# Kernel optimization log

Measured on AMD Instinct MI355X. Metric: run time of the kernel, lower is better.

The kernel has to match this reference:

```python
import jax, jax.numpy as jnp
import numpy as np

DN = ('NHWC', 'HWIO', 'NHWC')
EPS = 1e-3  # Keras BatchNormalization default epsilon


def conv2d(x, w):
    return jax.lax.conv_general_dilated(x, w, (1, 1), 'SAME', dimension_numbers=DN)


def hard_sigmoid(x):
    # Keras ConvLSTM2D default recurrent_activation
    return jnp.clip(0.2 * x + 0.5, 0.0, 1.0)


def convlstm2d(x, Wx, Wh, b):
    """Keras ConvLSTM2D, return_sequences=True. x: (B,T,H,W,C).
    Wx: (3,3,C,4F) input kernel, Wh: (3,3,F,4F) recurrent kernel, b: (4F,).
    Gate order (Keras): i, f, c, o."""
    B, T, H, W, C = x.shape
    F = Wh.shape[2]
    # input-to-gate convs for all timesteps in one batched conv
    xg = conv2d(x.reshape(B * T, H, W, C), Wx) + b          # (B*T,H,W,4F)
    xg = xg.reshape(B, T, H, W, 4 * F).transpose(1, 0, 2, 3, 4)  # (T,B,H,W,4F)

    def step(carry, xg_t):
        h, c = carry
        g = xg_t + conv2d(h, Wh)                            # (B,H,W,4F)
        i, f, cc, o = jnp.split(g, 4, axis=-1)
        i = hard_sigmoid(i)
        f = hard_sigmoid(f)
        o = hard_sigmoid(o)
        c = f * c + i * jnp.tanh(cc)
        h = o * jnp.tanh(c)
        return (h, c), h

    h0 = jnp.zeros((B, H, W, F), x.dtype)
    (_, _), hs = jax.lax.scan(step, (h0, h0), xg)           # hs: (T,B,H,W,F)
    return hs.transpose(1, 0, 2, 3, 4)


def batchnorm(x, gamma, beta):
    # training-mode BN over all axes except channel (last)
    mu = x.mean(axis=(0, 1, 2, 3), keepdims=True)
    var = x.var(axis=(0, 1, 2, 3), keepdims=True)
    return gamma * (x - mu) * jax.lax.rsqrt(var + EPS) + beta


def setup_inputs() -> dict:
    key = jax.random.key(0)
    B, T, H, W, C = 4, 8, 16, 16, 256
    F = 256
    ks = jax.random.split(key, 10)
    s = 0.02
    inp = {
        'input_tensor': jax.random.normal(ks[0], (B, T, H, W, C), jnp.float32),
        'Wx1': jax.random.normal(ks[1], (3, 3, C, 4 * F), jnp.float32) * s,
        'Wh1': jax.random.normal(ks[2], (3, 3, F, 4 * F), jnp.float32) * s,
        'b1': jnp.zeros((4 * F,), jnp.float32),
        'g1': jnp.ones((F,), jnp.float32),
        'be1': jnp.zeros((F,), jnp.float32),
        'Wx2': jax.random.normal(ks[3], (3, 3, F, 4 * F), jnp.float32) * s,
        'Wh2': jax.random.normal(ks[4], (3, 3, F, 4 * F), jnp.float32) * s,
        'b2': jnp.zeros((4 * F,), jnp.float32),
        'g2': jnp.ones((F,), jnp.float32),
        'be2': jnp.zeros((F,), jnp.float32),
        'Wx3': jax.random.normal(ks[5], (3, 3, F, 4 * F), jnp.float32) * s,
        'Wh3': jax.random.normal(ks[6], (3, 3, F, 4 * F), jnp.float32) * s,
        'b3': jnp.zeros((4 * F,), jnp.float32),
        'g3': jnp.ones((F,), jnp.float32),
        'be3': jnp.zeros((F,), jnp.float32),
    }
    return inp


def reference(input_tensor, Wx1, Wh1, b1, g1, be1,
              Wx2, Wh2, b2, g2, be2,
              Wx3, Wh3, b3, g3, be3):
    x = batchnorm(convlstm2d(input_tensor, Wx1, Wh1, b1), g1, be1)
    x = batchnorm(convlstm2d(x, Wx2, Wh2, b2), g2, be2)
    x = batchnorm(convlstm2d(x, Wx3, Wh3, b3), g3, be3)
    return x
```

## Files before the change

kernel.cpp:

```cpp
#include <hip/hip_runtime.h>

#define HW      256
#define COUT    1024
#define TSTEPS  8
#define BN_EPS  1e-3f
#define KTOT    2304

typedef unsigned short u16;
typedef unsigned int   u32;
typedef __attribute__((ext_vector_type(8))) _Float16 v8h;
typedef __attribute__((ext_vector_type(4))) float v4f;

__device__ __forceinline__ u16 f2h(float x) {
    _Float16 h = (_Float16)x; return *(u16*)&h;
}
__device__ __forceinline__ float h2f(u16 u) {
    _Float16 h = *(_Float16*)&u; return (float)h;
}
__device__ __forceinline__ float hsig(float x) {
    return fminf(fmaxf(0.2f * x + 0.5f, 0.f), 1.f);
}

typedef __attribute__((address_space(1))) const unsigned int gas_u32;
typedef __attribute__((address_space(3))) unsigned int las_u32;
__device__ __forceinline__ void gl16(const void* g, void* l) {
    __builtin_amdgcn_global_load_lds((gas_u32*)g, (las_u32*)l, 16, 0, 0);
}

__global__ __launch_bounds__(256, 2) void conv_big_k(
    const u16* __restrict__ apad,
    const u16* __restrict__ wT,
    const float* __restrict__ bias,
    u16* __restrict__ out)
{
    constexpr int KQ = 36;
    __shared__ u16 lds[2 * 16384];

    const int bid = blockIdx.x;
    const int xcd = bid & 7, idx = bid >> 3;
    const int by = (xcd >> 1) * 2 + (idx & 1);
    const int bx = (xcd & 1) * 32 + (idx >> 1);
    const int m0 = bx * 128, n0 = by * 128;
    const int tid = threadIdx.x, lane = tid & 63, w = tid >> 6;
    const int wr = w >> 1, wc = w & 1;
    const int lr = lane >> 3;
    const int g  = (lane & 7) ^ lr;
    const int fr = lane & 15, kc = lane >> 4;

    const char* a_src[4];
    #pragma unroll
    for (int i = 0; i < 4; ++i) {
        int m = m0 + w * 32 + i * 8 + lr;
        int img = m >> 8, pix = m & 255, yy = pix >> 4, xx = pix & 15;
        a_src[i] = (const char*)apad + ((((long)img * 18 + yy) * 18 + xx) * 256 + g * 8) * 2;
    }
    const char* b_src[4];
    #pragma unroll
    for (int i = 0; i < 4; ++i) {
        int n = n0 + w * 32 + i * 8 + lr;
        b_src[i] = (const char*)wT + ((long)n * KTOT + g * 8) * 2;
    }

    int aro[4][2], bro[4][2];
    #pragma unroll
    for (int mi = 0; mi < 4; ++mi) {
        int rl = wr * 64 + mi * 16 + fr;
        #pragma unroll
        for (int ks = 0; ks < 2; ++ks)
            aro[mi][ks] = rl * 128 + ((((ks << 2) | kc) ^ (fr & 7)) << 4);
    }
    #pragma unroll
    for (int ni = 0; ni < 4; ++ni) {
        int nr = wc * 64 + ni * 16 + fr;
        #pragma unroll
        for (int ks = 0; ks < 2; ++ks)
            bro[ni][ks] = 16384 + nr * 128 + ((((ks << 2) | kc) ^ (fr & 7)) << 4);
    }

    v4f acc[4][4];
    #pragma unroll
    for (int mi = 0; mi < 4; ++mi)
        #pragma unroll
        for (int ni = 0; ni < 4; ++ni) acc[mi][ni] = (v4f)0.f;

#define STAGE_B(J) { int j_ = (J); int dxy = j_ >> 2, c64 = j_ & 3;           \
    int dy = (dxy * 11) >> 5; int dx = dxy - dy * 3;                          \
    int aoff = ((dy * 18 + dx) * 256 + c64 * 64) * 2; int boff = j_ * 128;    \
    char* base = (char*)lds + (j_ & 1) * 32768;                               \
    _Pragma("unroll") for (int i = 0; i < 4; ++i)                             \
        gl16(a_src[i] + aoff, base + (w * 32 + i * 8) * 128);                 \
    _Pragma("unroll") for (int i = 0; i < 4; ++i)                             \
        gl16(b_src[i] + boff, base + 16384 + (w * 32 + i * 8) * 128); }

#define COMPUTE_B(J) { const char* base = (const char*)lds + ((J) & 1) * 32768; \
    v8h af[4][2], bf[4][2];                                                   \
    _Pragma("unroll") for (int mi = 0; mi < 4; ++mi)                          \
        _Pragma("unroll") for (int ks = 0; ks < 2; ++ks)                      \
            af[mi][ks] = *(const v8h*)(base + aro[mi][ks]);                   \
    _Pragma("unroll") for (int ni = 0; ni < 4; ++ni)                          \
        _Pragma("unroll") for (int ks = 0; ks < 2; ++ks)                      \
            bf[ni][ks] = *(const v8h*)(base + bro[ni][ks]);                   \
    __builtin_amdgcn_s_setprio(1);                                            \
    _Pragma("unroll") for (int ks = 0; ks < 2; ++ks)                          \
    _Pragma("unroll") for (int mi = 0; mi < 4; ++mi)                          \
    _Pragma("unroll") for (int ni = 0; ni < 4; ++ni)                          \
        acc[mi][ni] = __builtin_amdgcn_mfma_f32_16x16x32_f16(af[mi][ks], bf[ni][ks], acc[mi][ni], 0, 0, 0); \
    __builtin_amdgcn_s_setprio(0); }

    STAGE_B(0);
    for (int kq = 0; kq < KQ - 1; ++kq) {
        asm volatile("s_waitcnt vmcnt(0)" ::: "memory");
        __builtin_amdgcn_s_barrier();
        __builtin_amdgcn_sched_barrier(0);
        STAGE_B(kq + 1);
        COMPUTE_B(kq);
    }
    asm volatile("s_waitcnt vmcnt(0)" ::: "memory");
    __builtin_amdgcn_s_barrier();
    __builtin_amdgcn_sched_barrier(0);
    COMPUTE_B(KQ - 1);
#undef STAGE_B
#undef COMPUTE_B

    #pragma unroll
    for (int mi = 0; mi < 4; ++mi) {
        #pragma unroll
        for (int ni = 0; ni < 4; ++ni) {
            int mrow = m0 + wr * 64 + mi * 16 + ((lane >> 4) << 2);
            int ncol = n0 + wc * 64 + ni * 16 + fr;
            float b0 = bias[(ncol & 3) * 256 + (ncol >> 2)];
            #pragma unroll
            for (int r = 0; r < 4; ++r)
                out[(long)(mrow + r) * COUT + ncol] = f2h(acc[mi][ni][r] + b0);
        }
    }
}

__global__ __launch_bounds__(512) void rec_fused_k(
    const u16* __restrict__ ph_in,
    const u16* __restrict__ wTf,
    const u16* __restrict__ xg,
    float* __restrict__ cbuf,
    float* __restrict__ hs,
    u16* __restrict__ ph_out,
    int t)
{
    __shared__ u16 lds[6 * 4096];

    const int bid = blockIdx.x;
    const int by = (bid & 7) * 2 + ((bid >> 3) & 1);
    const int bx = bid >> 4;
    const int m0 = bx * 64, n0 = by * 64;
    const int tid = threadIdx.x, lane = tid & 63, w = tid >> 6;
    const int wr = w >> 2, wc = w & 3;
    const int fr = lane & 15, kc = lane >> 4;

    const int f4  = n0 + wc * 16 + (lane & 12);
    const int fch = f4 >> 2;
    int erow[2]; long xrow[2];
    uint2 xb_pre[2];
    #pragma unroll
    for (int mi = 0; mi < 2; ++mi) {
        erow[mi] = m0 + wr * 32 + mi * 16 + ((lane >> 4) << 2) + (lane & 3);
        int img = erow[mi] >> 8, pix = erow[mi] & 255;
        xrow[mi] = ((long)(img * TSTEPS + t) * HW + pix);
        xb_pre[mi] = *(const uint2*)&xg[xrow[mi] * COUT + f4];
    }

    const char* a_src;
    {
        int rt = tid >> 3;
        int gg = (tid & 7) ^ (rt & 7);
        int m = m0 + rt;
        int img = m >> 8, pix = m & 255, yy = pix >> 4, xx = pix & 15;
        a_src = (const char*)ph_in + ((((long)img * 18 + yy) * 18 + xx) * 256 + gg * 8) * 2;
    }
    const char* b_base = (const char*)wTf + ((long)(by * 4 + wc) * 72) * 1024 + lane * 16;

    int aro[2][2];
    #pragma unroll
    for (int mi = 0; mi < 2; ++mi)
        #pragma unroll
        for (int ks = 0; ks < 2; ++ks)
            aro[mi][ks] = (wr * 32 + mi * 16 + fr) * 128 + ((((ks << 2) | kc) ^ (fr & 7)) << 4);

    v4f acc0 = (v4f)0.f, acc1 = (v4f)0.f;

#define STAGE_A(J, BUF) { int j_ = (J); int dxy = j_ >> 2, c64 = j_ & 3;      \
    int dy = (dxy * 11) >> 5; int dx = dxy - dy * 3;                          \
    int aoff = ((dy * 18 + dx) * 256 + c64 * 64) * 2;                         \
    gl16(a_src + aoff, (char*)lds + (BUF) * 8192 + w * 1024); }

#define LDB(J, R0, R1) { R0 = *(const v8h*)(b_base + (2 * (J)) * 1024);       \
                         R1 = *(const v8h*)(b_base + (2 * (J) + 1) * 1024); }

#define CKQ(BUF, C0, C1) {                                                    \
    const char* base_ = (const char*)lds + (BUF) * 8192;                      \
    v8h af00_ = *(const v8h*)(base_ + aro[0][0]);                             \
    v8h af10_ = *(const v8h*)(base_ + aro[1][0]);                             \
    v8h af01_ = *(const v8h*)(base_ + aro[0][1]);                             \
    v8h af11_ = *(const v8h*)(base_ + aro[1][1]);                             \
    __builtin_amdgcn_s_setprio(1);                                            \
    acc0 = __builtin_amdgcn_mfma_f32_16x16x32_f16(af00_, C0, acc0, 0, 0, 0);  \
    acc1 = __builtin_amdgcn_mfma_f32_16x16x32_f16(af10_, C0, acc1, 0, 0, 0);  \
    acc0 = __builtin_amdgcn_mfma_f32_16x16x32_f16(af01_, C1, acc0, 0, 0, 0);  \
    acc1 = __builtin_amdgcn_mfma_f32_16x16x32_f16(af11_, C1, acc1, 0, 0, 0);  \
    __builtin_amdgcn_s_setprio(0); }

#define BODY2(J2, BC, BS, Ca0, Ca1, Cb0, Cb1, La0, La1, Lb0, Lb1) {           \
    int q0_ = 2 * (J2);                                                       \
    asm volatile("s_waitcnt vmcnt(6)" ::: "memory");                          \
    __builtin_amdgcn_s_barrier();                                             \
    __builtin_amdgcn_sched_barrier(0);                                        \
    LDB(q0_ + 4, La0, La1); LDB(q0_ + 5, Lb0, Lb1);                           \
    STAGE_A(q0_ + 4, BS); STAGE_A(q0_ + 5, (BS) + 1);                         \
    CKQ(BC,       Ca0, Ca1);                                                  \
    CKQ((BC) + 1, Cb0, Cb1); }

    v8h S00, S01, S02, S03, S10, S11, S12, S13, S20, S21, S22, S23;
    LDB(0, S00, S01); LDB(1, S02, S03); STAGE_A(0, 0); STAGE_A(1, 1);
    LDB(2, S10, S11); LDB(3, S12, S13); STAGE_A(2, 2); STAGE_A(3, 3);

    for (int j = 0; j < 5; ++j) {
        BODY2(3 * j,     0, 4, S00, S01, S02, S03, S20, S21, S22, S23);
        BODY2(3 * j + 1, 2, 0, S10, S11, S12, S13, S00, S01, S02, S03);
        BODY2(3 * j + 2, 4, 2, S20, S21, S22, S23, S10, S11, S12, S13);
    }
    BODY2(15, 0, 4, S00, S01, S02, S03, S20, S21, S22, S23);
    asm volatile("s_waitcnt vmcnt(6)" ::: "memory");
    __builtin_amdgcn_s_barrier();
    __builtin_amdgcn_sched_barrier(0);
    CKQ(2, S10, S11);
    CKQ(3, S12, S13);
    asm volatile("s_waitcnt vmcnt(0)" ::: "memory");
    __builtin_amdgcn_s_barrier();
    __builtin_amdgcn_sched_barrier(0);
    CKQ(4, S20, S21);
    CKQ(5, S22, S23);
#undef STAGE_A
#undef LDB
#undef CKQ
#undef BODY2

    v4f accA[2] = {acc0, acc1};
    const bool gl0 = lane & 1, gl1 = lane & 2;
    #pragma unroll
    for (int mi = 0; mi < 2; ++mi) {
        float V0 = accA[mi][0], V1 = accA[mi][1];
        float V2 = accA[mi][2], V3 = accA[mi][3];
        float x0 = __shfl_xor(V0, 1), x1 = __shfl_xor(V1, 1);
        float x2 = __shfl_xor(V2, 1), x3 = __shfl_xor(V3, 1);
        float a0 = gl0 ? x1 : V0;
        float a1 = gl0 ? V1 : x0;
        float a2 = gl0 ? x3 : V2;
        float a3 = gl0 ? V3 : x2;
        float s0 = __shfl_xor(a0, 2), s1 = __shfl_xor(a1, 2);
        float s2 = __shfl_xor(a2, 2), s3 = __shfl_xor(a3, 2);
        float Ti = gl1 ? s2 : a0;
        float Tf = gl1 ? s3 : a1;
        float Tc = gl1 ? a2 : s0;
        float To = gl1 ? a3 : s1;

        float pi = Ti + h2f((u16)(xb_pre[mi].x & 0xffff));
        float pf = Tf + h2f((u16)(xb_pre[mi].x >> 16));
        float pc = Tc + h2f((u16)(xb_pre[mi].y & 0xffff));
        float po = To + h2f((u16)(xb_pre[mi].y >> 16));
        long cidx = (long)erow[mi] * 256 + fch;
        float c = hsig(pf) * cbuf[cidx] + hsig(pi) * tanhf(pc);
        float h = hsig(po) * tanhf(c);
        cbuf[cidx] = c;
        hs[xrow[mi] * 256 + fch] = h;
        int pix = erow[mi] & 255, img = erow[mi] >> 8;
        ph_out[(((long)img * 18 + (pix >> 4) + 1) * 18 + (pix & 15) + 1) * 256 + fch] = f2h(h);
    }
}

__global__ __launch_bounds__(256) void gates0_k(
    const u16* __restrict__ xg, float* __restrict__ cbuf,
    float* __restrict__ hs, u16* __restrict__ ph_out)
{
    int idx = blockIdx.x * 256 + threadIdx.x;
    int fch = idx & 255, row = idx >> 8;
    int img = row >> 8, pix = row & 255;
    long xrow = (long)(img * TSTEPS) * HW + pix;
    uint2 xb = *(const uint2*)&xg[xrow * COUT + fch * 4];
    float pi = h2f((u16)(xb.x & 0xffff));
    float pc = h2f((u16)(xb.y & 0xffff));
    float po = h2f((u16)(xb.y >> 16));
    float c = hsig(pi) * tanhf(pc);
    float h = hsig(po) * tanhf(c);
    cbuf[(long)row * 256 + fch] = c;
    hs[xrow * 256 + fch] = h;
    int yy = pix >> 4, xx = pix & 15;
    ph_out[(((long)img * 18 + yy + 1) * 18 + xx + 1) * 256 + fch] = f2h(h);
}

__global__ __launch_bounds__(256) void wprep_all_k(
    const float* __restrict__ wx, const float* __restrict__ wh,
    u16* __restrict__ wT, u16* __restrict__ wTf)
{
    int kq = blockIdx.x;
    int by = blockIdx.y;
    if (by < 4) {
        int k0 = kq * 32;
        int np = by * 256 + threadIdx.x;
        int n  = (np & 3) * 256 + (np >> 2);
        u32 pk[16];
        #pragma unroll
        for (int kk = 0; kk < 32; kk += 2) {
            float a = wx[(long)(k0 + kk) * COUT + n];
            float b = wx[(long)(k0 + kk + 1) * COUT + n];
            pk[kk >> 1] = (u32)f2h(a) | ((u32)f2h(b) << 16);
        }
        uint4* dst = (uint4*)&wT[(long)np * KTOT + k0];
        dst[0] = make_uint4(pk[0], pk[1], pk[2], pk[3]);
        dst[1] = make_uint4(pk[4], pk[5], pk[6], pk[7]);
        dst[2] = make_uint4(pk[8], pk[9], pk[10], pk[11]);
        dst[3] = make_uint4(pk[12], pk[13], pk[14], pk[15]);
    } else {
        int nf = (by - 4) * 4 + (threadIdx.x >> 6);
        int l  = threadIdx.x & 63;
        int np = nf * 16 + (l & 15);
        int n  = (np & 3) * 256 + (np >> 2);
        int k0 = kq * 32 + (l >> 4) * 8;
        u32 pk[4];
        #pragma unroll
        for (int e = 0; e < 8; e += 2) {
            float a = wh[(long)(k0 + e) * COUT + n];
            float b = wh[(long)(k0 + e + 1) * COUT + n];
            pk[e >> 1] = (u32)f2h(a) | ((u32)f2h(b) << 16);
        }
        *(uint4*)&wTf[((long)(nf * 72) + kq) * 512 + l * 8] =
            make_uint4(pk[0], pk[1], pk[2], pk[3]);
    }
}

__global__ __launch_bounds__(256) void convert_x_k(const float* __restrict__ x,
                                                   u16* __restrict__ padx)
{
    int q = blockIdx.x * 256 + threadIdx.x;
    int e0 = q * 4;
    int f = e0 & 255, pix = (e0 >> 8) & 255, img = e0 >> 16;
    float4 v = ((const float4*)x)[q];
    int yy = pix >> 4, xx = pix & 15;
    long o = (((long)img * 18 + yy + 1) * 18 + xx + 1) * 256 + f;
    u32 lo = (u32)f2h(v.x) | ((u32)f2h(v.y) << 16);
    u32 hi = (u32)f2h(v.z) | ((u32)f2h(v.w) << 16);
    *(uint2*)&padx[o] = make_uint2(lo, hi);
}

__global__ __launch_bounds__(256) void bn_stats1_k(
    const float* __restrict__ x, float* __restrict__ partial)
{
    const int tid = threadIdx.x;
    const int blk = blockIdx.x;
    float s = 0.f, s2 = 0.f;
    const long base = (long)blk * 128 * 256;
    #pragma unroll 8
    for (int gi = 0; gi < 128; ++gi) {
        float v = x[base + gi * 256 + tid];
        s += v; s2 += v * v;
    }
    partial[blk * 512 + tid]       = s;
    partial[blk * 512 + 256 + tid] = s2;
}

__global__ __launch_bounds__(256) void bn_stats2_k(
    const float* __restrict__ partial, const float* __restrict__ gamma,
    const float* __restrict__ beta, float* __restrict__ stats)
{
    const int f = threadIdx.x;
    float s = 0.f, s2 = 0.f;
    #pragma unroll 8
    for (int b = 0; b < 64; ++b) {
        s  += partial[b * 512 + f];
        s2 += partial[b * 512 + 256 + f];
    }
    const float inv_n = 1.f / 8192.f;
    float mu  = s * inv_n;
    float var = s2 * inv_n - mu * mu;
    float sc  = gamma[f] * rsqrtf(var + BN_EPS);
    stats[f]       = sc;
    stats[256 + f] = beta[f] - mu * sc;
}

__global__ __launch_bounds__(256) void bn_apply_k(
    const float* __restrict__ x, const float* __restrict__ stats,
    u16* __restrict__ padx, float* __restrict__ out)
{
    const int q = blockIdx.x * 256 + threadIdx.x;
    const int e0 = q * 4;
    const int f = e0 & 255, pix = (e0 >> 8) & 255, img = e0 >> 16;
    float4 v  = ((const float4*)x)[q];
    float4 sc = *(const float4*)(stats + f);
    float4 sh = *(const float4*)(stats + 256 + f);
    v.x = v.x * sc.x + sh.x;
    v.y = v.y * sc.y + sh.y;
    v.z = v.z * sc.z + sh.z;
    v.w = v.w * sc.w + sh.w;
    if (out) ((float4*)out)[q] = v;
    if (padx) {
        int yy = pix >> 4, xx = pix & 15;
        long o = (((long)img * 18 + yy + 1) * 18 + xx + 1) * 256 + f;
        u32 lo = (u32)f2h(v.x) | ((u32)f2h(v.y) << 16);
        u32 hi = (u32)f2h(v.z) | ((u32)f2h(v.w) << 16);
        *(uint2*)&padx[o] = make_uint2(lo, hi);
    }
}

extern "C" void kernel_launch(void* const* d_in, const int* in_sizes, int n_in,
                              void* d_out, int out_size, void* d_ws, size_t ws_size,
                              hipStream_t stream)
{
    const float* x0    = (const float*)d_in[0];
    const float* Wx[3] = {(const float*)d_in[1], (const float*)d_in[6],  (const float*)d_in[11]};
    const float* Wh[3] = {(const float*)d_in[2], (const float*)d_in[7],  (const float*)d_in[12]};
    const float* bb[3] = {(const float*)d_in[3], (const float*)d_in[8],  (const float*)d_in[13]};
    const float* gg[3] = {(const float*)d_in[4], (const float*)d_in[9],  (const float*)d_in[14]};
    const float* be[3] = {(const float*)d_in[5], (const float*)d_in[10], (const float*)d_in[15]};

    float* ws    = (float*)d_ws;
    u16*  xg     = (u16*)ws;
    float* cbuf  = ws   + 4194304;
    float* hs    = cbuf + 262144;
    float* part  = hs   + 2097152;
    float* stats = part + 262144;
    u16*  pad_x  = (u16*)(stats + 512);
    u16*  pad_h  = pad_x + 2654208;
    u16*  wTx    = pad_h + 663552;
    u16*  wTf    = wTx   + 2359296;
    const long PHN = 331776;

    hipMemsetAsync(pad_x, 0, 2654208 * sizeof(u16), stream);
    hipMemsetAsync(pad_h, 0, 2 * PHN * sizeof(u16), stream);
    hipLaunchKernelGGL(convert_x_k, dim3(2048), dim3(256), 0, stream, x0, pad_x);

    for (int l = 0; l < 3; ++l) {
        hipLaunchKernelGGL(wprep_all_k, dim3(72, 20), dim3(256), 0, stream,
            Wx[l], Wh[l], wTx, wTf);

        hipLaunchKernelGGL(conv_big_k, dim3(512), dim3(256), 0, stream,
            pad_x, wTx, bb[l], xg);

        hipLaunchKernelGGL(gates0_k, dim3(1024), dim3(256), 0, stream,
            xg, cbuf, hs, pad_h + PHN);

        for (int t = 1; t < TSTEPS; ++t) {
            hipLaunchKernelGGL(rec_fused_k, dim3(256), dim3(512), 0, stream,
                pad_h + (t & 1) * PHN, wTf, xg, cbuf, hs,
                pad_h + ((t & 1) ^ 1) * PHN, t);
        }

        hipLaunchKernelGGL(bn_stats1_k, dim3(64), dim3(256), 0, stream, hs, part);
        hipLaunchKernelGGL(bn_stats2_k, dim3(1), dim3(256), 0, stream, part, gg[l], be[l], stats);
        hipLaunchKernelGGL(bn_apply_k, dim3(2048), dim3(256), 0, stream, hs, stats,
            (l < 2) ? pad_x : (u16*)nullptr, (l == 2) ? (float*)d_out : (float*)nullptr);
    }
}
```

Baseline: 471.3 us.

## Fuse t=0 gate computation into input conv epilogue and store hidden states in fp16

Removes the separate gates0 kernel by computing the first timestep's LSTM cell and hidden state inside the conv_big epilogue for blocks whose rows belong to t=0. The hidden-state sequence buffer changes from fp32 to fp16, which halves traffic in the BN stats and apply kernels. The BN stats partial grid is rebalanced to 128 blocks. The recurrent kernel also loads the previous cell state before the GEMM. The fp16 hidden-state storage slightly reduces the precision of the BN inputs.

```diff
diff --git a/kernel.cpp b/kernel.cpp
--- a/kernel.cpp
+++ b/kernel.cpp
@@ -31,7 +31,10 @@
     const u16* __restrict__ apad,
     const u16* __restrict__ wT,
     const float* __restrict__ bias,
-    u16* __restrict__ out)
+    u16* __restrict__ out,
+    float* __restrict__ cbuf,
+    u16* __restrict__ hs16,
+    u16* __restrict__ ph1)
 {
     constexpr int KQ = 36;
     __shared__ u16 lds[2 * 16384];
@@ -122,6 +125,8 @@
 #undef STAGE_B
 #undef COMPUTE_B
 
+    const bool t0blk = (((m0 >> 8) & 7) == 0);
+    const bool gl0 = lane & 1, gl1 = lane & 2;
     #pragma unroll
     for (int mi = 0; mi < 4; ++mi) {
         #pragma unroll
@@ -129,9 +134,36 @@
             int mrow = m0 + wr * 64 + mi * 16 + ((lane >> 4) << 2);
             int ncol = n0 + wc * 64 + ni * 16 + fr;
             float b0 = bias[(ncol & 3) * 256 + (ncol >> 2)];
-            #pragma unroll
-            for (int r = 0; r < 4; ++r)
-                out[(long)(mrow + r) * COUT + ncol] = f2h(acc[mi][ni][r] + b0);
+            float v0 = acc[mi][ni][0] + b0;
+            float v1 = acc[mi][ni][1] + b0;
+            float v2 = acc[mi][ni][2] + b0;
+            float v3 = acc[mi][ni][3] + b0;
+            out[(long)(mrow + 0) * COUT + ncol] = f2h(v0);
+            out[(long)(mrow + 1) * COUT + ncol] = f2h(v1);
+            out[(long)(mrow + 2) * COUT + ncol] = f2h(v2);
+            out[(long)(mrow + 3) * COUT + ncol] = f2h(v3);
+            if (t0blk) {
+                float x0 = __shfl_xor(v0, 1), x1 = __shfl_xor(v1, 1);
+                float x2 = __shfl_xor(v2, 1), x3 = __shfl_xor(v3, 1);
+                float a0 = gl0 ? x1 : v0;
+                float a1 = gl0 ? v1 : x0;
+                float a2 = gl0 ? x3 : v2;
+                float a3 = gl0 ? v3 : x2;
+                float s0 = __shfl_xor(a0, 2), s1 = __shfl_xor(a1, 2);
+                float s2 = __shfl_xor(a2, 2), s3 = __shfl_xor(a3, 2);
+                float Ti = gl1 ? s2 : a0;
+                float Tc = gl1 ? a2 : s0;
+                float To = gl1 ? a3 : s1;
+                int row = mrow + (lane & 3);
+                int fch = (n0 + wc * 64 + ni * 16 + (fr & 12)) >> 2;
+                float c = hsig(Ti) * tanhf(Tc);
+                float h = hsig(To) * tanhf(c);
+                int img = row >> 11, pix = row & 255;
+                u16 hv = f2h(h);
+                cbuf[((long)img * 256 + pix) * 256 + fch] = c;
+                hs16[(long)row * 256 + fch] = hv;
+                ph1[(((long)img * 18 + (pix >> 4) + 1) * 18 + (pix & 15) + 1) * 256 + fch] = hv;
+            }
         }
     }
 }
@@ -141,7 +173,7 @@
     const u16* __restrict__ wTf,
     const u16* __restrict__ xg,
     float* __restrict__ cbuf,
-    float* __restrict__ hs,
+    u16* __restrict__ hs16,
     u16* __restrict__ ph_out,
     int t)
 {
@@ -157,14 +189,17 @@
 
     const int f4  = n0 + wc * 16 + (lane & 12);
     const int fch = f4 >> 2;
-    int erow[2]; long xrow[2];
+    int erow[2]; long xrow[2], cidx[2];
     uint2 xb_pre[2];
+    float c_pre[2];
     #pragma unroll
     for (int mi = 0; mi < 2; ++mi) {
         erow[mi] = m0 + wr * 32 + mi * 16 + ((lane >> 4) << 2) + (lane & 3);
         int img = erow[mi] >> 8, pix = erow[mi] & 255;
         xrow[mi] = ((long)(img * TSTEPS + t) * HW + pix);
+        cidx[mi] = (long)erow[mi] * 256 + fch;
         xb_pre[mi] = *(const uint2*)&xg[xrow[mi] * COUT + f4];
+        c_pre[mi]  = cbuf[cidx[mi]];
     }
 
     const char* a_src;
@@ -265,34 +300,14 @@
         float pf = Tf + h2f((u16)(xb_pre[mi].x >> 16));
         float pc = Tc + h2f((u16)(xb_pre[mi].y & 0xffff));
         float po = To + h2f((u16)(xb_pre[mi].y >> 16));
-        long cidx = (long)erow[mi] * 256 + fch;
-        float c = hsig(pf) * cbuf[cidx] + hsig(pi) * tanhf(pc);
+        float c = hsig(pf) * c_pre[mi] + hsig(pi) * tanhf(pc);
         float h = hsig(po) * tanhf(c);
-        cbuf[cidx] = c;
-        hs[xrow[mi] * 256 + fch] = h;
+        cbuf[cidx[mi]] = c;
+        u16 hv = f2h(h);
+        hs16[xrow[mi] * 256 + fch] = hv;
         int pix = erow[mi] & 255, img = erow[mi] >> 8;
-        ph_out[(((long)img * 18 + (pix >> 4) + 1) * 18 + (pix & 15) + 1) * 256 + fch] = f2h(h);
-    }
-}
-
-__global__ __launch_bounds__(256) void gates0_k(
-    const u16* __restrict__ xg, float* __restrict__ cbuf,
-    float* __restrict__ hs, u16* __restrict__ ph_out)
-{
-    int idx = blockIdx.x * 256 + threadIdx.x;
-    int fch = idx & 255, row = idx >> 8;
-    int img = row >> 8, pix = row & 255;
-    long xrow = (long)(img * TSTEPS) * HW + pix;
-    uint2 xb = *(const uint2*)&xg[xrow * COUT + fch * 4];
-    float pi = h2f((u16)(xb.x & 0xffff));
-    float pc = h2f((u16)(xb.y & 0xffff));
-    float po = h2f((u16)(xb.y >> 16));
-    float c = hsig(pi) * tanhf(pc);
-    float h = hsig(po) * tanhf(c);
-    cbuf[(long)row * 256 + fch] = c;
-    hs[xrow * 256 + fch] = h;
-    int yy = pix >> 4, xx = pix & 15;
-    ph_out[(((long)img * 18 + yy + 1) * 18 + xx + 1) * 256 + fch] = f2h(h);
+        ph_out[(((long)img * 18 + (pix >> 4) + 1) * 18 + (pix & 15) + 1) * 256 + fch] = hv;
+    }
 }
 
 __global__ __launch_bounds__(256) void wprep_all_k(
@@ -350,15 +365,15 @@
 }
 
 __global__ __launch_bounds__(256) void bn_stats1_k(
-    const float* __restrict__ x, float* __restrict__ partial)
+    const u16* __restrict__ x, float* __restrict__ partial)
 {
     const int tid = threadIdx.x;
     const int blk = blockIdx.x;
     float s = 0.f, s2 = 0.f;
-    const long base = (long)blk * 128 * 256;
+    const long base = (long)blk * 64 * 256;
     #pragma unroll 8
-    for (int gi = 0; gi < 128; ++gi) {
-        float v = x[base + gi * 256 + tid];
+    for (int gi = 0; gi < 64; ++gi) {
+        float v = h2f(x[base + gi * 256 + tid]);
         s += v; s2 += v * v;
     }
     partial[blk * 512 + tid]       = s;
@@ -372,7 +387,7 @@
     const int f = threadIdx.x;
     float s = 0.f, s2 = 0.f;
     #pragma unroll 8
-    for (int b = 0; b < 64; ++b) {
+    for (int b = 0; b < 128; ++b) {
         s  += partial[b * 512 + f];
         s2 += partial[b * 512 + 256 + f];
     }
@@ -385,13 +400,14 @@
 }
 
 __global__ __launch_bounds__(256) void bn_apply_k(
-    const float* __restrict__ x, const float* __restrict__ stats,
+    const u16* __restrict__ x, const float* __restrict__ stats,
     u16* __restrict__ padx, float* __restrict__ out)
 {
     const int q = blockIdx.x * 256 + threadIdx.x;
     const int e0 = q * 4;
     const int f = e0 & 255, pix = (e0 >> 8) & 255, img = e0 >> 16;
-    float4 v  = ((const float4*)x)[q];
+    ushort4 hv = ((const ushort4*)x)[q];
+    float4 v = make_float4(h2f(hv.x), h2f(hv.y), h2f(hv.z), h2f(hv.w));
     float4 sc = *(const float4*)(stats + f);
     float4 sh = *(const float4*)(stats + 256 + f);
     v.x = v.x * sc.x + sh.x;
@@ -422,9 +438,9 @@
     float* ws    = (float*)d_ws;
     u16*  xg     = (u16*)ws;
     float* cbuf  = ws   + 4194304;
-    float* hs    = cbuf + 262144;
-    float* part  = hs   + 2097152;
-    float* stats = part + 262144;
+    u16*  hs16   = (u16*)(cbuf + 262144);
+    float* part  = (float*)(hs16 + 2097152);
+    float* stats = part + 65536;
     u16*  pad_x  = (u16*)(stats + 512);
     u16*  pad_h  = pad_x + 2654208;
     u16*  wTx    = pad_h + 663552;
@@ -440,20 +456,17 @@
             Wx[l], Wh[l], wTx, wTf);
 
         hipLaunchKernelGGL(conv_big_k, dim3(512), dim3(256), 0, stream,
-            pad_x, wTx, bb[l], xg);
-
-        hipLaunchKernelGGL(gates0_k, dim3(1024), dim3(256), 0, stream,
-            xg, cbuf, hs, pad_h + PHN);
+            pad_x, wTx, bb[l], xg, cbuf, hs16, pad_h + PHN);
 
         for (int t = 1; t < TSTEPS; ++t) {
             hipLaunchKernelGGL(rec_fused_k, dim3(256), dim3(512), 0, stream,
-                pad_h + (t & 1) * PHN, wTf, xg, cbuf, hs,
+                pad_h + (t & 1) * PHN, wTf, xg, cbuf, hs16,
                 pad_h + ((t & 1) ^ 1) * PHN, t);
         }
 
-        hipLaunchKernelGGL(bn_stats1_k, dim3(64), dim3(256), 0, stream, hs, part);
+        hipLaunchKernelGGL(bn_stats1_k, dim3(128), dim3(256), 0, stream, hs16, part);
         hipLaunchKernelGGL(bn_stats2_k, dim3(1), dim3(256), 0, stream, part, gg[l], be[l], stats);
-        hipLaunchKernelGGL(bn_apply_k, dim3(2048), dim3(256), 0, stream, hs, stats,
+        hipLaunchKernelGGL(bn_apply_k, dim3(2048), dim3(256), 0, stream, hs16, stats,
             (l < 2) ? pad_x : (u16*)nullptr, (l == 2) ? (float*)d_out : (float*)nullptr);
     }
 }
```

After: 483.0 us. 2.5% more time.
